# Optimization experiments

Measured on AMD Instinct MI355X. Metric: run time of the kernel, lower is better.

## Reference

```python
import jax, jax.numpy as jnp
import numpy as np

VOCAB, EMBED, HID = 32000, 512, 1024
B, S = 64, 512


def setup_inputs() -> dict:
    key = jax.random.key(0)
    ks = jax.random.split(key, 14)
    sc = lambda fan: 1.0 / np.sqrt(fan)
    return {
        "input_token": jax.random.randint(ks[0], (B, 1), 0, VOCAB),
        "h": jax.random.normal(ks[1], (1, B, HID), jnp.float32),
        "c": jax.random.normal(ks[2], (1, B, HID), jnp.float32),
        "encoder_outputs": jax.random.normal(ks[3], (B, S, HID), jnp.float32),
        "emb": jax.random.normal(ks[4], (VOCAB, EMBED), jnp.float32).at[0].set(0.0),
        "W1": jax.random.normal(ks[5], (HID, HID), jnp.float32) * sc(HID),
        "W2": jax.random.normal(ks[6], (HID, HID), jnp.float32) * sc(HID),
        "v": jax.random.normal(ks[7], (HID,), jnp.float32) * sc(HID),
        "W_ih": jax.random.normal(ks[8], (4 * HID, EMBED + HID), jnp.float32) * sc(EMBED + HID),
        "W_hh": jax.random.normal(ks[9], (4 * HID, HID), jnp.float32) * sc(HID),
        "b_ih": jax.random.normal(ks[10], (4 * HID,), jnp.float32) * 0.01,
        "b_hh": jax.random.normal(ks[11], (4 * HID,), jnp.float32) * 0.01,
        "fc_W": jax.random.normal(ks[12], (VOCAB, 2 * HID), jnp.float32) * sc(2 * HID),
        "fc_b": jax.random.normal(ks[13], (VOCAB,), jnp.float32) * 0.01,
    }


def reference(input_token, h, c, encoder_outputs, emb, W1, W2, v,
              W_ih, W_hh, b_ih, b_hh, fc_W, fc_b):
    # Embedding (dropout = identity in eval)
    embedded = emb[input_token[:, 0]]                       # [B, E]
    h0 = h[0]                                               # [B, H]
    c0 = c[0]                                               # [B, H]

    # Bahdanau additive attention
    dh = h0 @ W1.T                                          # [B, H]
    eh = jnp.einsum('bsh,kh->bsk', encoder_outputs, W2)     # [B, S, H]
    energy = jnp.tanh(dh[:, None, :] + eh)                  # [B, S, H]
    scores = jnp.einsum('bsh,h->bs', energy, v)             # [B, S]
    attn = jax.nn.softmax(scores, axis=-1)                  # [B, S]
    context = jnp.einsum('bs,bsh->bh', attn, encoder_outputs)  # [B, H]

    # Single LSTM step (PyTorch gate order: i, f, g, o)
    x = jnp.concatenate([embedded, context], axis=-1)       # [B, E+H]
    gates = x @ W_ih.T + b_ih + h0 @ W_hh.T + b_hh          # [B, 4H]
    i, f, g, o = jnp.split(gates, 4, axis=-1)
    c1 = jax.nn.sigmoid(f) * c0 + jax.nn.sigmoid(i) * jnp.tanh(g)
    h1 = jax.nn.sigmoid(o) * jnp.tanh(c1)                   # [B, H]

    # Output projection
    out = jnp.concatenate([h1, context], axis=-1)           # [B, 2H]
    prediction = out @ fc_W.T + fc_b                        # [B, V]
    return prediction, (h1[None], c1[None]), attn
```

## Files before the change

### kernel.cpp

```cpp
#include <hip/hip_runtime.h>
#include <math.h>

#define VOCAB 32000
#define EMBED 512
#define HID   1024
#define BATCH 64
#define SEQ   512

#define OUT_H1   2048000
#define OUT_C1   2113536
#define OUT_ATTN 2179072

typedef __bf16 bf16x8 __attribute__((ext_vector_type(8)));
typedef float  f32x4  __attribute__((ext_vector_type(4)));

__device__ __forceinline__ unsigned short f2bf(float f) {
  unsigned int u = __builtin_bit_cast(unsigned int, f);
  u += 0x7fffu + ((u >> 16) & 1u);
  return (unsigned short)(u >> 16);
}
__device__ __forceinline__ float bf2f(unsigned int u) {
  return __builtin_bit_cast(float, u << 16);
}

__device__ __forceinline__ float fast_tanh(float x) {
  float cx = fminf(fmaxf(x, -15.f), 15.f);
  float t = __builtin_amdgcn_exp2f(cx * 2.8853900817779268f);
  return (t - 1.f) / (t + 1.f);
}

__device__ __forceinline__ void gload16(const unsigned short* g, unsigned short* l) {
  __builtin_amdgcn_global_load_lds(
      (const __attribute__((address_space(1))) void*)g,
      (__attribute__((address_space(3))) void*)l, 16, 0, 0);
}

__device__ __forceinline__ void stage16(const float* __restrict__ src, unsigned short* dst) {
  float4 f0 = *(const float4*)(src + 0);
  float4 f1 = *(const float4*)(src + 4);
  float4 f2 = *(const float4*)(src + 8);
  float4 f3 = *(const float4*)(src + 12);
  union { unsigned short us[16]; uint4 u4[2]; } p;
  p.us[0]=f2bf(f0.x);  p.us[1]=f2bf(f0.y);  p.us[2]=f2bf(f0.z);  p.us[3]=f2bf(f0.w);
  p.us[4]=f2bf(f1.x);  p.us[5]=f2bf(f1.y);  p.us[6]=f2bf(f1.z);  p.us[7]=f2bf(f1.w);
  p.us[8]=f2bf(f2.x);  p.us[9]=f2bf(f2.y);  p.us[10]=f2bf(f2.z); p.us[11]=f2bf(f2.w);
  p.us[12]=f2bf(f3.x); p.us[13]=f2bf(f3.y); p.us[14]=f2bf(f3.z); p.us[15]=f2bf(f3.w);
  *(uint4*)(dst + 0) = p.u4[0];
  *(uint4*)(dst + 8) = p.u4[1];
}

__global__ void zero_ws_kernel(float* __restrict__ p) {
  int i = blockIdx.x * 256 + threadIdx.x;
  *(float4*)(p + (size_t)i * 4) = (float4){0.f, 0.f, 0.f, 0.f};
}

__global__ void f2bf_kernel(const float* __restrict__ src, unsigned short* __restrict__ dst,
                            int n8) {
  int i = blockIdx.x * blockDim.x + threadIdx.x;
  int stride = gridDim.x * blockDim.x;
  for (; i < n8; i += stride) {
    const float* s = src + (size_t)i * 8;
    float4 f0 = *(const float4*)s;
    float4 f1 = *(const float4*)(s + 4);
    union { unsigned short us[8]; uint4 u; } p;
    p.us[0]=f2bf(f0.x); p.us[1]=f2bf(f0.y); p.us[2]=f2bf(f0.z); p.us[3]=f2bf(f0.w);
    p.us[4]=f2bf(f1.x); p.us[5]=f2bf(f1.y); p.us[6]=f2bf(f1.z); p.us[7]=f2bf(f1.w);
    *(uint4*)(dst + (size_t)i * 8) = p.u;
  }
}

__global__ void dh_w2_kernel(const float* __restrict__ h0, const float* __restrict__ W1,
                             float* __restrict__ dh,
                             const float* __restrict__ W2, unsigned short* __restrict__ W2b) {
  __shared__ float hs[HID];
  int bid = blockIdx.x, t = threadIdx.x;
  if (bid < 256) {
    int b = bid >> 2, kblk = bid & 3;
    for (int i = t; i < HID; i += 256) hs[i] = h0[b * HID + i];
    __syncthreads();
    int k = kblk * 256 + t;
    const float* w = W1 + (size_t)k * HID;
    float acc = 0.f;
    for (int hh = 0; hh < HID; hh += 4) {
      float4 wv = *(const float4*)(w + hh);
      float4 hv = *(const float4*)(hs + hh);
      acc += wv.x * hv.x + wv.y * hv.y + wv.z * hv.z + wv.w * hv.w;
    }
    dh[b * HID + k] = acc;
  } else {
    int i = (bid - 256) * 256 + t;
    const float* s = W2 + (size_t)i * 8;
    float4 f0 = *(const float4*)s;
    float4 f1 = *(const float4*)(s + 4);
    union { unsigned short us[8]; uint4 u; } p;
    p.us[0]=f2bf(f0.x); p.us[1]=f2bf(f0.y); p.us[2]=f2bf(f0.z); p.us[3]=f2bf(f0.w);
    p.us[4]=f2bf(f1.x); p.us[5]=f2bf(f1.y); p.us[6]=f2bf(f1.z); p.us[7]=f2bf(f1.w);
    *(uint4*)(W2b + (size_t)i * 8) = p.u;
  }
}

__launch_bounds__(512, 2)
__global__ void scores8_kernel(const unsigned short* __restrict__ encb,
                               const unsigned short* __restrict__ W2b,
                               const float* __restrict__ dh, const float* __restrict__ v,
                               float* __restrict__ scores) {
  __shared__ __align__(16) unsigned short sA[2][16384];
  __shared__ __align__(16) unsigned short sB[2][16384];
  __shared__ float dh_s[256];
  __shared__ float v_s[256];

  int bid = blockIdx.x;
  int wg = (bid & 7) * 64 + (bid >> 3);
  int mt = wg >> 2, nt = wg & 3;
  int m0 = mt * 256, n0 = nt * 256;

  int t = threadIdx.x;
  int wid = t >> 6, l = t & 63;
  int wr = wid >> 2, wc = wid & 3;
  int fr = l & 15, co = (l >> 4) * 8;

  const unsigned short* pa0;
  const unsigned short* pb0;
  int do0 = wid * 512;
  {
    int row0 = wid * 8 + (l >> 3);
    int colE = ((l & 7) ^ ((l >> 3) & 7)) << 3;
    pa0 = encb + (size_t)(m0 + row0) * HID + colE;
    pb0 = W2b + (size_t)(n0 + row0) * HID + colE;
  }

  f32x4 acc[8][4];
#pragma unroll
  for (int i = 0; i < 8; i++)
#pragma unroll
    for (int j = 0; j < 4; j++) acc[i][j] = (f32x4){0.f, 0.f, 0.f, 0.f};

#define SC_STAGE(T, d)                                                         \
  do {                                                                         \
    int k0_ = (T) * 64;                                                        \
    gload16(pa0 + k0_,          &sA[d][do0]);                                  \
    gload16(pa0 + 65536 + k0_,  &sA[d][do0 + 4096]);                           \
    gload16(pa0 + 131072 + k0_, &sA[d][do0 + 8192]);                           \
    gload16(pa0 + 196608 + k0_, &sA[d][do0 + 12288]);                          \
    gload16(pb0 + k0_,          &sB[d][do0]);                                  \
    gload16(pb0 + 65536 + k0_,  &sB[d][do0 + 4096]);                           \
    gload16(pb0 + 131072 + k0_, &sB[d][do0 + 8192]);                           \
    gload16(pb0 + 196608 + k0_, &sB[d][do0 + 12288]);                          \
  } while (0)

  SC_STAGE(0, 0);
  SC_STAGE(1, 1);

#define LDF(Mat, row, ks) \
  (*(const bf16x8*)&Mat[(row) * 64 + (((ks) * 32 + co) ^ (((row) & 7) << 3))])

  for (int T = 0; T < 16; ++T) {
    int d = T & 1;
    if (T == 15) asm volatile("s_waitcnt vmcnt(0)" ::: "memory");
    else         asm volatile("s_waitcnt vmcnt(8)" ::: "memory");
    asm volatile("s_barrier" ::: "memory");
    const unsigned short* A = sA[d];
    const unsigned short* B = sB[d];
    bf16x8 a[4][2], b[4][2];
#pragma unroll
    for (int jj = 0; jj < 4; ++jj)
#pragma unroll
      for (int ks = 0; ks < 2; ++ks)
        b[jj][ks] = LDF(B, wc * 64 + jj * 16 + fr, ks);
#pragma unroll
    for (int ii = 0; ii < 4; ++ii)
#pragma unroll
      for (int ks = 0; ks < 2; ++ks)
        a[ii][ks] = LDF(A, wr * 128 + ii * 16 + fr, ks);
    __builtin_amdgcn_s_setprio(1);
#pragma unroll
    for (int ii = 0; ii < 4; ++ii)
#pragma unroll
      for (int jj = 0; jj < 2; ++jj)
#pragma unroll
        for (int ks = 0; ks < 2; ++ks)
          acc[ii][jj] = __builtin_amdgcn_mfma_f32_16x16x32_bf16(a[ii][ks], b[jj][ks], acc[ii][jj], 0, 0, 0);
    __builtin_amdgcn_s_setprio(0);
    __builtin_amdgcn_s_setprio(1);
#pragma unroll
    for (int ii = 0; ii < 4; ++ii)
#pragma unroll
      for (int jj = 2; jj < 4; ++jj)
#pragma unroll
        for (int ks = 0; ks < 2; ++ks)
          acc[ii][jj] = __builtin_amdgcn_mfma_f32_16x16x32_bf16(a[ii][ks], b[jj][ks], acc[ii][jj], 0, 0, 0);
    __builtin_amdgcn_s_setprio(0);
#pragma unroll
    for (int ii = 0; ii < 4; ++ii)
#pragma unroll
      for (int ks = 0; ks < 2; ++ks)
        a[ii][ks] = LDF(A, wr * 128 + 64 + ii * 16 + fr, ks);
    __builtin_amdgcn_s_setprio(1);
#pragma unroll
    for (int ii = 0; ii < 4; ++ii)
#pragma unroll
      for (int jj = 2; jj < 4; ++jj)
#pragma unroll
        for (int ks = 0; ks < 2; ++ks)
          acc[4 + ii][jj] = __builtin_amdgcn_mfma_f32_16x16x32_bf16(a[ii][ks], b[jj][ks], acc[4 + ii][jj], 0, 0, 0);
    __builtin_amdgcn_s_setprio(0);
    __builtin_amdgcn_s_setprio(1);
#pragma unroll
    for (int ii = 0; ii < 4; ++ii)
#pragma unroll
      for (int jj = 0; jj < 2; ++jj)
#pragma unroll
        for (int ks = 0; ks < 2; ++ks)
          acc[4 + ii][jj] = __builtin_amdgcn_mfma_f32_16x16x32_bf16(a[ii][ks], b[jj][ks], acc[4 + ii][jj], 0, 0, 0);
    __builtin_amdgcn_s_setprio(0);
    asm volatile("s_barrier" ::: "memory");
    if (T < 14) SC_STAGE(T + 2, d);
  }
#undef LDF
#undef SC_STAGE

  int b = m0 >> 9;
  if (t < 256) { dh_s[t] = dh[b * HID + n0 + t]; v_s[t] = v[n0 + t]; }
  __syncthreads();
  float sp[32];
#pragma unroll
  for (int q = 0; q < 32; ++q) sp[q] = 0.f;
#pragma unroll
  for (int ii = 0; ii < 8; ++ii)
#pragma unroll
    for (int jj = 0; jj < 4; ++jj) {
      int nl = wc * 64 + jj * 16 + fr;
      float dv = dh_s[nl], vv = v_s[nl];
#pragma unroll
      for (int r = 0; r < 4; ++r)
        sp[ii * 4 + r] += fast_tanh(dv + acc[ii][jj][r]) * vv;
    }
#pragma unroll
  for (int q = 0; q < 32; ++q) {
    float x = sp[q];
    x += __shfl_xor(x, 1);
    x += __shfl_xor(x, 2);
    x += __shfl_xor(x, 4);
    x += __shfl_xor(x, 8);
    sp[q] = x;
  }
  if (fr == 0) {
    int rbase = m0 + wr * 128 + (l >> 4) * 4;
#pragma unroll
    for (int ii = 0; ii < 8; ++ii)
#pragma unroll
      for (int r = 0; r < 4; ++r)
        atomicAdd(&scores[rbase + ii * 16 + r], sp[ii * 4 + r]);
  }
}

__global__ void softmax_kernel(const float* __restrict__ scores, float* __restrict__ attn) {
  __shared__ float red[8];
  int b = blockIdx.x, t = threadIdx.x;
  float x = scores[b * SEQ + t];
  float m = x;
  for (int d = 1; d < 64; d <<= 1) m = fmaxf(m, __shfl_xor(m, d));
  if ((t & 63) == 0) red[t >> 6] = m;
  __syncthreads();
  float bm = red[0];
#pragma unroll
  for (int i = 1; i < 8; i++) bm = fmaxf(bm, red[i]);
  float e = expf(x - bm);
  float s = e;
  for (int d = 1; d < 64; d <<= 1) s += __shfl_xor(s, d);
  __syncthreads();
  if ((t & 63) == 0) red[t >> 6] = s;
  __syncthreads();
  float bs = 0.f;
#pragma unroll
  for (int i = 0; i < 8; i++) bs += red[i];
  attn[b * SEQ + t] = e / bs;
}

__global__ void context2_kernel(const unsigned short* __restrict__ encb,
                                const float* __restrict__ attn, float* __restrict__ ctx) {
  __shared__ float a_s[64];
  int b = blockIdx.y, s0 = blockIdx.x * 64, t = threadIdx.x;
  if (t < 64) a_s[t] = attn[b * SEQ + s0 + t];
  __syncthreads();
  int hg = (t & 127) * 8, sg = (t >> 7) * 32;
  float a0 = 0.f, a1 = 0.f, a2 = 0.f, a3 = 0.f, a4 = 0.f, a5 = 0.f, a6 = 0.f, a7 = 0.f;
  const unsigned short* base = encb + ((size_t)b * SEQ + s0 + sg) * HID + hg;
  for (int s = 0; s < 32; s++) {
    uint4 ev = *(const uint4*)(base + (size_t)s * HID);
    float a = a_s[sg + s];
    a0 += a * bf2f(ev.x & 0xffffu); a1 += a * bf2f(ev.x >> 16);
    a2 += a * bf2f(ev.y & 0xffffu); a3 += a * bf2f(ev.y >> 16);
    a4 += a * bf2f(ev.z & 0xffffu); a5 += a * bf2f(ev.z >> 16);
    a6 += a * bf2f(ev.w & 0xffffu); a7 += a * bf2f(ev.w >> 16);
  }
  atomicAdd(&ctx[b * HID + hg + 0], a0);
  atomicAdd(&ctx[b * HID + hg + 1], a1);
  atomicAdd(&ctx[b * HID + hg + 2], a2);
  atomicAdd(&ctx[b * HID + hg + 3], a3);
  atomicAdd(&ctx[b * HID + hg + 4], a4);
  atomicAdd(&ctx[b * HID + hg + 5], a5);
  atomicAdd(&ctx[b * HID + hg + 6], a6);
  atomicAdd(&ctx[b * HID + hg + 7], a7);
}

__launch_bounds__(256)
__global__ void gates8p_kernel(const int* __restrict__ tok, const float* __restrict__ emb,
                               const float* __restrict__ ctx, const float* __restrict__ h0,
                               const float* __restrict__ W_ih, const float* __restrict__ W_hh,
                               float* __restrict__ gpart) {
  __shared__ __align__(16) unsigned short lA[64 * 40];
  __shared__ __align__(16) unsigned short lB[128 * 40];
  int n0 = blockIdx.x * 128, kz = blockIdx.y;
  int kbase = kz * 320;
  int t = threadIdx.x, w = t >> 6, l = t & 63;
  f32x4 acc[4][2];
#pragma unroll
  for (int i = 0; i < 4; i++)
#pragma unroll
    for (int j = 0; j < 2; j++) acc[i][j] = (f32x4){0.f, 0.f, 0.f, 0.f};
  int rowA = t >> 2, qA = (t & 3) * 8;
  int rowB = t >> 1, hB = t & 1;
  int tkA = tok[rowA];

  for (int kt = 0; kt < 10; kt++) {
    int k0 = kbase + kt * 32;
    {
      int kg = k0 + qA;
      const float* src;
      if (kg < 512)        src = emb + (size_t)tkA * EMBED + kg;
      else if (kg < 1536)  src = ctx + rowA * HID + (kg - 512);
      else                 src = h0 + rowA * HID + (kg - 1536);
      float4 f0 = *(const float4*)src;
      float4 f1 = *(const float4*)(src + 4);
      union { unsigned short us[8]; uint4 u; } p;
      p.us[0]=f2bf(f0.x); p.us[1]=f2bf(f0.y); p.us[2]=f2bf(f0.z); p.us[3]=f2bf(f0.w);
      p.us[4]=f2bf(f1.x); p.us[5]=f2bf(f1.y); p.us[6]=f2bf(f1.z); p.us[7]=f2bf(f1.w);
      *(uint4*)&lA[rowA * 40 + qA] = p.u;
    }
    {
      int kg = k0 + hB * 16;
      const float* src = (kg < 1536) ? (W_ih + (size_t)(n0 + rowB) * 1536 + kg)
                                     : (W_hh + (size_t)(n0 + rowB) * 1024 + (kg - 1536));
      stage16(src, &lB[rowB * 40 + hB * 16]);
    }
    __syncthreads();
    bf16x8 af[4], bv[2];
    int co = (l >> 4) * 8;
#pragma unroll
    for (int i = 0; i < 4; i++) af[i] = *(const bf16x8*)&lA[(i * 16 + (l & 15)) * 40 + co];
#pragma unroll
    for (int j = 0; j < 2; j++) bv[j] = *(const bf16x8*)&lB[(w * 32 + j * 16 + (l & 15)) * 40 + co];
#pragma unroll
    for (int i = 0; i < 4; i++)
#pragma unroll
      for (int j = 0; j < 2; j++)
        acc[i][j] = __builtin_amdgcn_mfma_f32_16x16x32_bf16(af[i], bv[j], acc[i][j], 0, 0, 0);
    __syncthreads();
  }
#pragma unroll
  for (int i = 0; i < 4; i++)
#pragma unroll
    for (int j = 0; j < 2; j++) {
      int n = n0 + w * 32 + j * 16 + (l & 15);
#pragma unroll
      for (int r = 0; r < 4; r++) {
        int m = i * 16 + (l >> 4) * 4 + r;
        gpart[(size_t)kz * 262144 + (size_t)m * 4096 + n] = acc[i][j][r];
      }
    }
}

__global__ void lstm_kernel(const float* __restrict__ gpart, const float* __restrict__ b_ih,
                            const float* __restrict__ b_hh, const float* __restrict__ c0,
                            float* __restrict__ out) {
  int b = blockIdx.y;
  int hh = blockIdx.x * 256 + threadIdx.x;
  float gi = b_ih[hh]        + b_hh[hh];
  float gf = b_ih[1024 + hh] + b_hh[1024 + hh];
  float gg = b_ih[2048 + hh] + b_hh[2048 + hh];
  float go = b_ih[3072 + hh] + b_hh[3072 + hh];
#pragma unroll
  for (int kz = 0; kz < 8; kz++) {
    const float* g = gpart + (size_t)kz * 262144 + (size_t)b * 4096;
    gi += g[hh];
    gf += g[1024 + hh];
    gg += g[2048 + hh];
    go += g[3072 + hh];
  }
  float si = 1.f / (1.f + expf(-gi));
  float sf = 1.f / (1.f + expf(-gf));
  float so = 1.f / (1.f + expf(-go));
  float c1 = sf * c0[b * HID + hh] + si * tanhf(gg);
  float h1 = so * tanhf(c1);
  out[OUT_H1 + b * HID + hh] = h1;
  out[OUT_C1 + b * HID + hh] = c1;
}

__launch_bounds__(256)
__global__ void fc2p_kernel(const float* __restrict__ h1, const float* __restrict__ ctx,
                            const float* __restrict__ fcW, float* __restrict__ part) {
  __shared__ __align__(16) unsigned short lA[64 * 40];
  __shared__ __align__(16) unsigned short lB[128 * 40];
  int n0 = blockIdx.x * 128, kz = blockIdx.y;
  const float* A = kz ? ctx : h1;
  int t = threadIdx.x, w = t >> 6, l = t & 63;
  f32x4 acc[4][2];
#pragma unroll
  for (int i = 0; i < 4; i++)
#pragma unroll
    for (int j = 0; j < 2; j++) acc[i][j] = (f32x4){0.f, 0.f, 0.f, 0.f};
  int rowA = t >> 2, qA = (t & 3) * 8;
  int rowB = t >> 1, hB = t & 1;

  for (int kt = 0; kt < 32; kt++) {
    int k0 = kt * 32;
    {
      const float* src = A + rowA * HID + k0 + qA;
      float4 f0 = *(const float4*)src;
      float4 f1 = *(const float4*)(src + 4);
      union { unsigned short us[8]; uint4 u; } p;
      p.us[0]=f2bf(f0.x); p.us[1]=f2bf(f0.y); p.us[2]=f2bf(f0.z); p.us[3]=f2bf(f0.w);
      p.us[4]=f2bf(f1.x); p.us[5]=f2bf(f1.y); p.us[6]=f2bf(f1.z); p.us[7]=f2bf(f1.w);
      *(uint4*)&lA[rowA * 40 + qA] = p.u;
    }
    stage16(fcW + (size_t)(n0 + rowB) * 2048 + kz * 1024 + k0 + hB * 16,
            &lB[rowB * 40 + hB * 16]);
    __syncthreads();
    bf16x8 af[4], bv[2];
    int co = (l >> 4) * 8;
#pragma unroll
    for (int i = 0; i < 4; i++) af[i] = *(const bf16x8*)&lA[(i * 16 + (l & 15)) * 40 + co];
#pragma unroll
    for (int j = 0; j < 2; j++) bv[j] = *(const bf16x8*)&lB[(w * 32 + j * 16 + (l & 15)) * 40 + co];
#pragma unroll
    for (int i = 0; i < 4; i++)
#pragma unroll
      for (int j = 0; j < 2; j++)
        acc[i][j] = __builtin_amdgcn_mfma_f32_16x16x32_bf16(af[i], bv[j], acc[i][j], 0, 0, 0);
    __syncthreads();
  }
#pragma unroll
  for (int i = 0; i < 4; i++)
#pragma unroll
    for (int j = 0; j < 2; j++) {
      int n = n0 + w * 32 + j * 16 + (l & 15);
#pragma unroll
      for (int r = 0; r < 4; r++) {
        int m = i * 16 + (l >> 4) * 4 + r;
        part[(size_t)kz * 2048000 + (size_t)m * VOCAB + n] = acc[i][j][r];
      }
    }
}

__global__ void fc_combine_kernel(const float* __restrict__ part,
                                  const float* __restrict__ fcb, float* __restrict__ pred) {
  int i = blockIdx.x * 256 + threadIdx.x;
  int m = i / 8000, n4 = i % 8000;
  size_t e = (size_t)m * VOCAB + n4 * 4;
  float4 p0 = *(const float4*)(part + e);
  float4 p1 = *(const float4*)(part + 2048000 + e);
  float4 bb = *(const float4*)(fcb + n4 * 4);
  float4 o;
  o.x = p0.x + p1.x + bb.x;
  o.y = p0.y + p1.y + bb.y;
  o.z = p0.z + p1.z + bb.z;
  o.w = p0.w + p1.w + bb.w;
  *(float4*)(pred + e) = o;
}

extern "C" void kernel_launch(void* const* d_in, const int* in_sizes, int n_in,
                              void* d_out, int out_size, void* d_ws, size_t ws_size,
                              hipStream_t stream) {
  const int*   tok  = (const int*)d_in[0];
  const float* h    = (const float*)d_in[1];
  const float* c    = (const float*)d_in[2];
  const float* enc  = (const float*)d_in[3];
  const float* emb  = (const float*)d_in[4];
  const float* W1   = (const float*)d_in[5];
  const float* W2   = (const float*)d_in[6];
  const float* v    = (const float*)d_in[7];
  const float* W_ih = (const float*)d_in[8];
  const float* W_hh = (const float*)d_in[9];
  const float* b_ih = (const float*)d_in[10];
  const float* b_hh = (const float*)d_in[11];
  const float* fcW  = (const float*)d_in[12];
  const float* fcb  = (const float*)d_in[13];
  float* out = (float*)d_out;

  float* wsf    = (float*)d_ws;
  float* scores = wsf;
  float* ctx    = wsf + 32768;
  float* dh     = wsf + 98304;
  float* gpart  = wsf + 163840;
  float* part   = wsf + 2260992;
  unsigned short* encb = (unsigned short*)(wsf + 6356992);
  unsigned short* W2b  = encb + (size_t)BATCH * SEQ * HID;

  zero_ws_kernel<<<96, 256, 0, stream>>>(wsf);
  f2bf_kernel<<<2048, 256, 0, stream>>>(enc, encb, BATCH * SEQ * HID / 8);
  dh_w2_kernel<<<768, 256, 0, stream>>>(h, W1, dh, W2, W2b);
  scores8_kernel<<<512, 512, 0, stream>>>(encb, W2b, dh, v, scores);
  softmax_kernel<<<64, 512, 0, stream>>>(scores, out + OUT_ATTN);
  context2_kernel<<<dim3(8, 64), 256, 0, stream>>>(encb, out + OUT_ATTN, ctx);
  gates8p_kernel<<<dim3(32, 8), 256, 0, stream>>>(tok, emb, ctx, h, W_ih, W_hh, gpart);
  lstm_kernel<<<dim3(4, 64), 256, 0, stream>>>(gpart, b_ih, b_hh, c, out);
  fc2p_kernel<<<dim3(250, 2), 256, 0, stream>>>(out + OUT_H1, ctx, fcW, part);
  fc_combine_kernel<<<2000, 256, 0, stream>>>(part, fcb, out);
}
```

Before: 292.9 us.

## Replace score atomics with per-N-tile partials, drop zero kernel, narrow FC tiles

The scores kernel now reduces its four column-warps through shared memory and writes one partial per N-tile into a separate buffer, instead of issuing global atomicAdds. The softmax kernel sums the four partials and also zeroes the context buffer, so the separate workspace-zeroing launch is removed. The FC projection kernel switches from 128-wide to 64-wide N tiles, doubling its grid to 1000 blocks for better occupancy, at the cost of re-reading the A operand more often. This also adds an extra __syncthreads and 4KB of shared memory in the scores kernel.

```diff
diff --git a/kernel.cpp b/kernel.cpp
--- a/kernel.cpp
+++ b/kernel.cpp
@@ -33,25 +33,6 @@
   __builtin_amdgcn_global_load_lds(
       (const __attribute__((address_space(1))) void*)g,
       (__attribute__((address_space(3))) void*)l, 16, 0, 0);
-}
-
-__device__ __forceinline__ void stage16(const float* __restrict__ src, unsigned short* dst) {
-  float4 f0 = *(const float4*)(src + 0);
-  float4 f1 = *(const float4*)(src + 4);
-  float4 f2 = *(const float4*)(src + 8);
-  float4 f3 = *(const float4*)(src + 12);
-  union { unsigned short us[16]; uint4 u4[2]; } p;
-  p.us[0]=f2bf(f0.x);  p.us[1]=f2bf(f0.y);  p.us[2]=f2bf(f0.z);  p.us[3]=f2bf(f0.w);
-  p.us[4]=f2bf(f1.x);  p.us[5]=f2bf(f1.y);  p.us[6]=f2bf(f1.z);  p.us[7]=f2bf(f1.w);
-  p.us[8]=f2bf(f2.x);  p.us[9]=f2bf(f2.y);  p.us[10]=f2bf(f2.z); p.us[11]=f2bf(f2.w);
-  p.us[12]=f2bf(f3.x); p.us[13]=f2bf(f3.y); p.us[14]=f2bf(f3.z); p.us[15]=f2bf(f3.w);
-  *(uint4*)(dst + 0) = p.u4[0];
-  *(uint4*)(dst + 8) = p.u4[1];
-}
-
-__global__ void zero_ws_kernel(float* __restrict__ p) {
-  int i = blockIdx.x * 256 + threadIdx.x;
-  *(float4*)(p + (size_t)i * 4) = (float4){0.f, 0.f, 0.f, 0.f};
 }
 
 __global__ void f2bf_kernel(const float* __restrict__ src, unsigned short* __restrict__ dst,
@@ -103,11 +84,12 @@
 __global__ void scores8_kernel(const unsigned short* __restrict__ encb,
                                const unsigned short* __restrict__ W2b,
                                const float* __restrict__ dh, const float* __restrict__ v,
-                               float* __restrict__ scores) {
+                               float* __restrict__ spart) {
   __shared__ __align__(16) unsigned short sA[2][16384];
   __shared__ __align__(16) unsigned short sB[2][16384];
   __shared__ float dh_s[256];
   __shared__ float v_s[256];
+  __shared__ float red4[4][256];
 
   int bid = blockIdx.x;
   int wg = (bid & 7) * 64 + (bid >> 3);
@@ -245,19 +227,24 @@
     sp[q] = x;
   }
   if (fr == 0) {
-    int rbase = m0 + wr * 128 + (l >> 4) * 4;
+    int rl = wr * 128 + (l >> 4) * 4;
 #pragma unroll
     for (int ii = 0; ii < 8; ++ii)
 #pragma unroll
       for (int r = 0; r < 4; ++r)
-        atomicAdd(&scores[rbase + ii * 16 + r], sp[ii * 4 + r]);
-  }
-}
-
-__global__ void softmax_kernel(const float* __restrict__ scores, float* __restrict__ attn) {
+        red4[wc][rl + ii * 16 + r] = sp[ii * 4 + r];
+  }
+  __syncthreads();
+  if (t < 256)
+    spart[nt * 32768 + m0 + t] = red4[0][t] + red4[1][t] + red4[2][t] + red4[3][t];
+}
+
+__global__ void softmax_kernel(const float* __restrict__ spart, float* __restrict__ attn,
+                               float* __restrict__ ctx) {
   __shared__ float red[8];
   int b = blockIdx.x, t = threadIdx.x;
-  float x = scores[b * SEQ + t];
+  int row = b * SEQ + t;
+  float x = spart[row] + spart[32768 + row] + spart[65536 + row] + spart[98304 + row];
   float m = x;
   for (int d = 1; d < 64; d <<= 1) m = fmaxf(m, __shfl_xor(m, d));
   if ((t & 63) == 0) red[t >> 6] = m;
@@ -275,6 +262,8 @@
 #pragma unroll
   for (int i = 0; i < 8; i++) bs += red[i];
   attn[b * SEQ + t] = e / bs;
+  ctx[b * HID + t] = 0.f;
+  ctx[b * HID + 512 + t] = 0.f;
 }
 
 __global__ void context2_kernel(const unsigned short* __restrict__ encb,
@@ -342,7 +331,17 @@
       int kg = k0 + hB * 16;
       const float* src = (kg < 1536) ? (W_ih + (size_t)(n0 + rowB) * 1536 + kg)
                                      : (W_hh + (size_t)(n0 + rowB) * 1024 + (kg - 1536));
-      stage16(src, &lB[rowB * 40 + hB * 16]);
+      float4 f0 = *(const float4*)src;
+      float4 f1 = *(const float4*)(src + 4);
+      float4 f2 = *(const float4*)(src + 8);
+      float4 f3 = *(const float4*)(src + 12);
+      union { unsigned short us[16]; uint4 u4[2]; } p;
+      p.us[0]=f2bf(f0.x);  p.us[1]=f2bf(f0.y);  p.us[2]=f2bf(f0.z);  p.us[3]=f2bf(f0.w);
+      p.us[4]=f2bf(f1.x);  p.us[5]=f2bf(f1.y);  p.us[6]=f2bf(f1.z);  p.us[7]=f2bf(f1.w);
+      p.us[8]=f2bf(f2.x);  p.us[9]=f2bf(f2.y);  p.us[10]=f2bf(f2.z); p.us[11]=f2bf(f2.w);
+      p.us[12]=f2bf(f3.x); p.us[13]=f2bf(f3.y); p.us[14]=f2bf(f3.z); p.us[15]=f2bf(f3.w);
+      *(uint4*)&lB[rowB * 40 + hB * 16 + 0] = p.u4[0];
+      *(uint4*)&lB[rowB * 40 + hB * 16 + 8] = p.u4[1];
     }
     __syncthreads();
     bf16x8 af[4], bv[2];
@@ -398,59 +397,59 @@
 }
 
 __launch_bounds__(256)
-__global__ void fc2p_kernel(const float* __restrict__ h1, const float* __restrict__ ctx,
+__global__ void fc64_kernel(const float* __restrict__ h1, const float* __restrict__ ctx,
                             const float* __restrict__ fcW, float* __restrict__ part) {
   __shared__ __align__(16) unsigned short lA[64 * 40];
-  __shared__ __align__(16) unsigned short lB[128 * 40];
-  int n0 = blockIdx.x * 128, kz = blockIdx.y;
+  __shared__ __align__(16) unsigned short lB[64 * 40];
+  int n0 = blockIdx.x * 64, kz = blockIdx.y;
   const float* A = kz ? ctx : h1;
   int t = threadIdx.x, w = t >> 6, l = t & 63;
-  f32x4 acc[4][2];
-#pragma unroll
-  for (int i = 0; i < 4; i++)
-#pragma unroll
-    for (int j = 0; j < 2; j++) acc[i][j] = (f32x4){0.f, 0.f, 0.f, 0.f};
-  int rowA = t >> 2, qA = (t & 3) * 8;
-  int rowB = t >> 1, hB = t & 1;
+  int fr = l & 15;
+  f32x4 acc[4];
+#pragma unroll
+  for (int i = 0; i < 4; i++) acc[i] = (f32x4){0.f, 0.f, 0.f, 0.f};
+  int rowS = t >> 2, qS = (t & 3) * 8;
 
   for (int kt = 0; kt < 32; kt++) {
     int k0 = kt * 32;
     {
-      const float* src = A + rowA * HID + k0 + qA;
+      const float* src = A + rowS * HID + k0 + qS;
       float4 f0 = *(const float4*)src;
       float4 f1 = *(const float4*)(src + 4);
       union { unsigned short us[8]; uint4 u; } p;
       p.us[0]=f2bf(f0.x); p.us[1]=f2bf(f0.y); p.us[2]=f2bf(f0.z); p.us[3]=f2bf(f0.w);
       p.us[4]=f2bf(f1.x); p.us[5]=f2bf(f1.y); p.us[6]=f2bf(f1.z); p.us[7]=f2bf(f1.w);
-      *(uint4*)&lA[rowA * 40 + qA] = p.u;
-    }
-    stage16(fcW + (size_t)(n0 + rowB) * 2048 + kz * 1024 + k0 + hB * 16,
-            &lB[rowB * 40 + hB * 16]);
+      *(uint4*)&lA[rowS * 40 + qS] = p.u;
+    }
+    {
+      const float* src = fcW + (size_t)(n0 + rowS) * 2048 + kz * 1024 + k0 + qS;
+      float4 f0 = *(const float4*)src;
+      float4 f1 = *(const float4*)(src + 4);
+      union { unsigned short us[8]; uint4 u; } p;
+      p.us[0]=f2bf(f0.x); p.us[1]=f2bf(f0.y); p.us[2]=f2bf(f0.z); p.us[3]=f2bf(f0.w);
+      p.us[4]=f2bf(f1.x); p.us[5]=f2bf(f1.y); p.us[6]=f2bf(f1.z); p.us[7]=f2bf(f1.w);
+      *(uint4*)&lB[rowS * 40 + qS] = p.u;
+    }
     __syncthreads();
-    bf16x8 af[4], bv[2];
+    bf16x8 af[4], bv;
     int co = (l >> 4) * 8;
 #pragma unroll
-    for (int i = 0; i < 4; i++) af[i] = *(const bf16x8*)&lA[(i * 16 + (l & 15)) * 40 + co];
-#pragma unroll
-    for (int j = 0; j < 2; j++) bv[j] = *(const bf16x8*)&lB[(w * 32 + j * 16 + (l & 15)) * 40 + co];
+    for (int i = 0; i < 4; i++) af[i] = *(const bf16x8*)&lA[(i * 16 + fr) * 40 + co];
+    bv = *(const bf16x8*)&lB[(w * 16 + fr) * 40 + co];
 #pragma unroll
     for (int i = 0; i < 4; i++)
-#pragma unroll
-      for (int j = 0; j < 2; j++)
-        acc[i][j] = __builtin_amdgcn_mfma_f32_16x16x32_bf16(af[i], bv[j], acc[i][j], 0, 0, 0);
+      acc[i] = __builtin_amdgcn_mfma_f32_16x16x32_bf16(af[i], bv, acc[i], 0, 0, 0);
     __syncthreads();
   }
 #pragma unroll
-  for (int i = 0; i < 4; i++)
-#pragma unroll
-    for (int j = 0; j < 2; j++) {
-      int n = n0 + w * 32 + j * 16 + (l & 15);
-#pragma unroll
-      for (int r = 0; r < 4; r++) {
-        int m = i * 16 + (l >> 4) * 4 + r;
-        part[(size_t)kz * 2048000 + (size_t)m * VOCAB + n] = acc[i][j][r];
-      }
-    }
+  for (int i = 0; i < 4; i++) {
+    int n = n0 + w * 16 + fr;
+#pragma unroll
+    for (int r = 0; r < 4; r++) {
+      int m = i * 16 + (l >> 4) * 4 + r;
+      part[(size_t)kz * 2048000 + (size_t)m * VOCAB + n] = acc[i][r];
+    }
+  }
 }
 
 __global__ void fc_combine_kernel(const float* __restrict__ part,
@@ -489,22 +488,21 @@
   float* out = (float*)d_out;
 
   float* wsf    = (float*)d_ws;
-  float* scores = wsf;
-  float* ctx    = wsf + 32768;
-  float* dh     = wsf + 98304;
-  float* gpart  = wsf + 163840;
-  float* part   = wsf + 2260992;
-  unsigned short* encb = (unsigned short*)(wsf + 6356992);
+  float* spart  = wsf;
+  float* ctx    = wsf + 131072;
+  float* dh     = wsf + 196608;
+  float* gpart  = wsf + 262144;
+  float* part   = wsf + 2359296;
+  unsigned short* encb = (unsigned short*)(wsf + 6455296);
   unsigned short* W2b  = encb + (size_t)BATCH * SEQ * HID;
 
-  zero_ws_kernel<<<96, 256, 0, stream>>>(wsf);
   f2bf_kernel<<<2048, 256, 0, stream>>>(enc, encb, BATCH * SEQ * HID / 8);
   dh_w2_kernel<<<768, 256, 0, stream>>>(h, W1, dh, W2, W2b);
-  scores8_kernel<<<512, 512, 0, stream>>>(encb, W2b, dh, v, scores);
-  softmax_kernel<<<64, 512, 0, stream>>>(scores, out + OUT_ATTN);
+  scores8_kernel<<<512, 512, 0, stream>>>(encb, W2b, dh, v, spart);
+  softmax_kernel<<<64, 512, 0, stream>>>(spart, out + OUT_ATTN, ctx);
   context2_kernel<<<dim3(8, 64), 256, 0, stream>>>(encb, out + OUT_ATTN, ctx);
   gates8p_kernel<<<dim3(32, 8), 256, 0, stream>>>(tok, emb, ctx, h, W_ih, W_hh, gpart);
   lstm_kernel<<<dim3(4, 64), 256, 0, stream>>>(gpart, b_ih, b_hh, c, out);
-  fc2p_kernel<<<dim3(250, 2), 256, 0, stream>>>(out + OUT_H1, ctx, fcW, part);
+  fc64_kernel<<<dim3(500, 2), 256, 0, stream>>>(out + OUT_H1, ctx, fcW, part);
   fc_combine_kernel<<<2000, 256, 0, stream>>>(part, fcb, out);
 }
```

After: 271.2 us. -7.4%, faster.
